# Kernel tuning notes

Measured on AMD Instinct MI355X. Metric: run time of the kernel, lower is better.

## Reference

```python
import jax, jax.numpy as jnp
import numpy as np

NEG_BIG = -1e38

def setup_inputs() -> dict:
    key = jax.random.key(0)
    kq, kk, kv, kwq, kwk = jax.random.split(key, 5)
    B, S, d_model, d_k, d_v = 4, 4096, 256, 64, 64
    return {
        "q": jax.random.normal(kq, (B, S, d_model), dtype=jnp.float32),
        "k": jax.random.normal(kk, (B, S, d_model), dtype=jnp.float32),
        "v": jax.random.normal(kv, (B, S, d_v), dtype=jnp.float32),
        "w_q": jax.random.normal(kwq, (d_k, d_model), dtype=jnp.float32) * 0.01,
        "w_k": jax.random.normal(kwk, (d_k, d_model), dtype=jnp.float32) * 0.01,
    }

def reference(q, k, v, w_q, w_k):
    d_k = w_q.shape[0]
    temperature = jnp.asarray(np.power(d_k, 0.5), dtype=q.dtype)
    # relu-projected Q, K: [B,S,d_k]
    qp = jax.nn.relu(jnp.einsum("bsm,km->bsk", q, w_q))
    kp = jax.nn.relu(jnp.einsum("bsm,km->bsk", k, w_k))
    # scores [B,S,S]
    attn = jnp.einsum("bqd,bkd->bqk", qp, kp) / temperature
    # force column 0 to -1e38 (inline custom mask)
    attn = attn.at[:, :, 0].set(NEG_BIG)
    attn = jax.nn.softmax(attn, axis=2)
    # dropout is identity in eval / p=0
    out = jnp.einsum("bqk,bkd->bqd", attn, v)
    return out
```

## Files before the change

### kernel.cpp

```cpp
#include <hip/hip_runtime.h>

#define B_    4
#define S_    4096
#define DM    256
#define DK    64
#define NROWS (B_ * S_)
#define LOG2E 1.4426950408889634f
#define PACK_BIAS 0.0028151295f

typedef __attribute__((ext_vector_type(8))) short bfrag;
typedef __attribute__((ext_vector_type(4))) float ffrag;

__device__ __forceinline__ unsigned bf16_rne_hi(float x) {
    unsigned u = __float_as_uint(x);
    return u + 0x7fffu + ((u >> 16) & 1u);
}
__device__ __forceinline__ unsigned short f2bf(float x) {
    return (unsigned short)(bf16_rne_hi(x) >> 16);
}
__device__ __forceinline__ unsigned pack_bf16x2(float lo, float hi) {
    return (bf16_rne_hi(hi) & 0xffff0000u) | (bf16_rne_hi(lo) >> 16);
}

__device__ __forceinline__ float fast_exp2(float x) {
#if __has_builtin(__builtin_amdgcn_exp2f)
    return __builtin_amdgcn_exp2f(x);
#else
    float r;
    asm("v_exp_f32 %0, %1\n\ts_nop 1" : "=v"(r) : "v"(x));
    return r;
#endif
}

__device__ __forceinline__ unsigned trunc_pack_bf16x2(float lo, float hi) {
    return __builtin_amdgcn_perm(__float_as_uint(hi), __float_as_uint(lo),
                                 0x07060302u);
}

__global__ __launch_bounds__(256) void fused_prep(
    const float* __restrict__ q, const float* __restrict__ k,
    const float* __restrict__ v, const float* __restrict__ wq,
    const float* __restrict__ wk, unsigned short* __restrict__ vT,
    unsigned short* __restrict__ qpb, unsigned short* __restrict__ kpb)
{
    __shared__ __align__(16) char smem[64 * 264 * 2];
    const int blk  = blockIdx.x;
    const int lane = threadIdx.x & 63, w = threadIdx.x >> 6;

    if (blk < 256) {
        float (*tile)[65] = (float(*)[65])smem;
        const int b = blk >> 6, s0 = (blk & 63) * 64;
#pragma unroll
        for (int i = 0; i < 16; ++i) {
            const int sl = i * 4 + w;
            tile[sl][lane] = v[(b * S_ + s0 + sl) * DK + lane];
        }
        __syncthreads();
        const int t32 = lane >> 5, pos = lane & 31;
        const int keyl = t32 * 32 + ((pos & 1) ? (pos >> 1) + 16 : (pos >> 1));
#pragma unroll
        for (int i = 0; i < 16; ++i) {
            const int d = i * 4 + w;
            vT[((size_t)(b * 128 + (s0 >> 5) + t32) * 64 + d) * 32 + pos] =
                f2bf(tile[keyl][d]);
        }
    } else {
        unsigned short* wlds = (unsigned short*)smem;
        const int pb = blk - 256;
        const int half = pb >> 8, rblk = pb & 255;
        const float* x;
        const float* wsrc;
        unsigned short* o;
        float scale;
        if (half == 0) { x = q; wsrc = wq; o = qpb; scale = 0.125f * LOG2E; }
        else           { x = k; wsrc = wk; o = kpb; scale = 1.0f; }

#pragma unroll
        for (int i = 0; i < 16; ++i) {
            const int idx4 = i * 256 + threadIdx.x;
            const int r = idx4 >> 6, c4 = idx4 & 63;
            const float4 wv = ((const float4*)wsrc)[idx4];
            uint2 pk;
            pk.x = pack_bf16x2(wv.x, wv.y);
            pk.y = pack_bf16x2(wv.z, wv.w);
            *(uint2*)&wlds[r * 264 + c4 * 4] = pk;
        }
        __syncthreads();

        const int m = lane & 15, quad = lane >> 4;
        const int rows0 = rblk * 64 + w * 16;
        const float* xrow = x + (size_t)(rows0 + m) * DM + quad * 8;

        ffrag acc[4];
#pragma unroll
        for (int dt = 0; dt < 4; ++dt) acc[dt] = (ffrag)(0.0f);

        float4 xb[2][2];
        xb[0][0] = ((const float4*)xrow)[0];
        xb[0][1] = ((const float4*)xrow)[1];

#pragma unroll 2
        for (int kf = 0; kf < 8; ++kf) {
            const int p = kf & 1;
            if (kf < 7) {
                const float4* xn = (const float4*)(xrow + (kf + 1) * 32);
                xb[p ^ 1][0] = xn[0];
                xb[p ^ 1][1] = xn[1];
            }
            union { bfrag v; unsigned u[4]; } pk;
            pk.u[0] = pack_bf16x2(xb[p][0].x, xb[p][0].y);
            pk.u[1] = pack_bf16x2(xb[p][0].z, xb[p][0].w);
            pk.u[2] = pack_bf16x2(xb[p][1].x, xb[p][1].y);
            pk.u[3] = pack_bf16x2(xb[p][1].z, xb[p][1].w);
#pragma unroll
            for (int dt = 0; dt < 4; ++dt) {
                const bfrag Bf = *(const bfrag*)&wlds[(dt * 16 + m) * 264 + kf * 32 + quad * 8];
                acc[dt] = __builtin_amdgcn_mfma_f32_16x16x32_bf16(pk.v, Bf, acc[dt], 0, 0, 0);
            }
        }
#pragma unroll
        for (int dt = 0; dt < 4; ++dt)
#pragma unroll
            for (int r = 0; r < 4; ++r)
                o[(rows0 + quad * 4 + r) * DK + dt * 16 + m] =
                    f2bf(fmaxf(acc[dt][r], 0.0f) * scale);
    }
}

__global__ __launch_bounds__(256) void attn_mfma(
    const unsigned short* __restrict__ qp, const unsigned short* __restrict__ kp,
    const unsigned short* __restrict__ vT, float* __restrict__ num_part,
    float* __restrict__ den_part)
{
    __shared__ __align__(16) char smem[20480];
    unsigned short* Plds = (unsigned short*)smem;
    float* red0 = (float*)smem;
    float* red1 = (float*)smem + 2560;

    const int lane = threadIdx.x & 63, w = threadIdx.x >> 6;
    const int m = lane & 15, quad = lane >> 4;

    const int flat = blockIdx.x;
    const int wid  = ((flat & 7) << 7) | (flat >> 3);
    const int gy   = wid & 1;
    const int qg   = wid >> 1;

    const int qbase = qg * 32;
    const int b = qg >> 7;
    const int kstart = (gy * 4 + w) * 512;

    bfrag qa[2][2];
#pragma unroll
    for (int mt = 0; mt < 2; ++mt)
#pragma unroll
        for (int kf = 0; kf < 2; ++kf)
            qa[mt][kf] = *(const bfrag*)&qp[(qbase + mt * 16 + m) * DK + kf * 32 + quad * 8];

    ffrag oacc[2][4];
    float dacc[2][4];
#pragma unroll
    for (int mt = 0; mt < 2; ++mt) {
#pragma unroll
        for (int dt = 0; dt < 4; ++dt) oacc[mt][dt] = (ffrag)(0.0f);
#pragma unroll
        for (int r = 0; r < 4; ++r) dacc[mt][r] = 0.0f;
    }

    const unsigned short* kptr = kp + ((size_t)b * S_ + kstart + m) * DK + quad * 8;
    const unsigned short* vptr = vT + ((size_t)(b * 128 + (kstart >> 5)) * 64 + m) * 32 + quad * 8;
    unsigned short* Pw = Plds + w * 1280;

    const ffrag cbias = (ffrag)(PACK_BIAS);

    bfrag kbuf[2][2][2], vbuf[2][4];
#pragma unroll
    for (int kt = 0; kt < 2; ++kt)
#pragma unroll
        for (int kf = 0; kf < 2; ++kf)
            kbuf[0][kt][kf] = *(const bfrag*)(kptr + kt * 1024 + kf * 32);
#pragma unroll
    for (int dt = 0; dt < 4; ++dt)
        vbuf[0][dt] = *(const bfrag*)(vptr + dt * 512);

    bfrag pa0, pa1;

#pragma unroll 2
    for (int jj = 0; jj < 16; ++jj) {
        const int p = jj & 1;

        if (jj < 15) {
            const unsigned short* kn = kptr + (jj + 1) * 2048;
#pragma unroll
            for (int kt = 0; kt < 2; ++kt)
#pragma unroll
                for (int kf = 0; kf < 2; ++kf)
                    kbuf[p ^ 1][kt][kf] = *(const bfrag*)(kn + kt * 1024 + kf * 32);
        }

        if (jj > 0) {
#pragma unroll
            for (int dt = 0; dt < 4; ++dt) {
                oacc[0][dt] = __builtin_amdgcn_mfma_f32_16x16x32_bf16(pa0, vbuf[p ^ 1][dt], oacc[0][dt], 0, 0, 0);
                oacc[1][dt] = __builtin_amdgcn_mfma_f32_16x16x32_bf16(pa1, vbuf[p ^ 1][dt], oacc[1][dt], 0, 0, 0);
            }
        }

        if (jj < 15) {
            const unsigned short* vn = vptr + (jj + 1) * 2048;
#pragma unroll
            for (int dt = 0; dt < 4; ++dt)
                vbuf[p ^ 1][dt] = *(const bfrag*)(vn + dt * 512);
        }

        ffrag s[2][2];
#pragma unroll
        for (int mt = 0; mt < 2; ++mt)
#pragma unroll
            for (int kt = 0; kt < 2; ++kt) {
                ffrag t = __builtin_amdgcn_mfma_f32_16x16x32_bf16(qa[mt][0], kbuf[p][kt][0], cbias, 0, 0, 0);
                s[mt][kt] = __builtin_amdgcn_mfma_f32_16x16x32_bf16(qa[mt][1], kbuf[p][kt][1], t, 0, 0, 0);
            }

        const bool mask0 = (jj == 0) && (kstart == 0) && (m == 0);
#pragma unroll
        for (int mt = 0; mt < 2; ++mt)
#pragma unroll
            for (int r = 0; r < 4; ++r) {
                float e0 = fast_exp2(s[mt][0][r]);
                float e1 = fast_exp2(s[mt][1][r]);
                if (mask0) e0 = 0.0f;
                dacc[mt][r] += e0 + e1;
                *(unsigned*)&Pw[(mt * 16 + quad * 4 + r) * 40 + m * 2] =
                    trunc_pack_bf16x2(e0, e1);
            }

        pa0 = *(const bfrag*)&Pw[(m) * 40 + quad * 8];
        pa1 = *(const bfrag*)&Pw[(16 + m) * 40 + quad * 8];
    }
#pragma unroll
    for (int dt = 0; dt < 4; ++dt) {
        oacc[0][dt] = __builtin_amdgcn_mfma_f32_16x16x32_bf16(pa0, vbuf[1][dt], oacc[0][dt], 0, 0, 0);
        oacc[1][dt] = __builtin_amdgcn_mfma_f32_16x16x32_bf16(pa1, vbuf[1][dt], oacc[1][dt], 0, 0, 0);
    }

#pragma unroll
    for (int mt = 0; mt < 2; ++mt)
#pragma unroll
        for (int r = 0; r < 4; ++r) {
            float d = dacc[mt][r];
            d += __shfl_xor(d, 1, 64);
            d += __shfl_xor(d, 2, 64);
            d += __shfl_xor(d, 4, 64);
            d += __shfl_xor(d, 8, 64);
            dacc[mt][r] = d;
        }

    __syncthreads();
    float* red[2] = { red0, red1 };
    if (w >= 2) {
#pragma unroll
        for (int mt = 0; mt < 2; ++mt) {
#pragma unroll
            for (int dt = 0; dt < 4; ++dt)
#pragma unroll
                for (int r = 0; r < 4; ++r)
                    red[w - 2][((mt * 4 + dt) * 4 + r) * 64 + lane] = oacc[mt][dt][r];
#pragma unroll
            for (int r = 0; r < 4; ++r)
                red[w - 2][2048 + (mt * 4 + r) * 64 + lane] = dacc[mt][r];
        }
    }
    __syncthreads();
    if (w < 2) {
#pragma unroll
        for (int mt = 0; mt < 2; ++mt) {
#pragma unroll
            for (int dt = 0; dt < 4; ++dt)
#pragma unroll
                for (int r = 0; r < 4; ++r)
                    oacc[mt][dt][r] += red[w][((mt * 4 + dt) * 4 + r) * 64 + lane];
#pragma unroll
            for (int r = 0; r < 4; ++r)
                dacc[mt][r] += red[w][2048 + (mt * 4 + r) * 64 + lane];
        }
    }
    __syncthreads();
    if (w == 1) {
#pragma unroll
        for (int mt = 0; mt < 2; ++mt) {
#pragma unroll
            for (int dt = 0; dt < 4; ++dt)
#pragma unroll
                for (int r = 0; r < 4; ++r)
                    red0[((mt * 4 + dt) * 4 + r) * 64 + lane] = oacc[mt][dt][r];
#pragma unroll
            for (int r = 0; r < 4; ++r)
                red0[2048 + (mt * 4 + r) * 64 + lane] = dacc[mt][r];
        }
    }
    __syncthreads();
    if (w == 0) {
#pragma unroll
        for (int mt = 0; mt < 2; ++mt) {
#pragma unroll
            for (int dt = 0; dt < 4; ++dt)
#pragma unroll
                for (int r = 0; r < 4; ++r) {
                    const float nv = oacc[mt][dt][r] + red0[((mt * 4 + dt) * 4 + r) * 64 + lane];
                    num_part[(size_t)gy * NROWS * DK +
                             (qbase + mt * 16 + quad * 4 + r) * DK + dt * 16 + m] = nv;
                }
#pragma unroll
            for (int r = 0; r < 4; ++r) {
                const float dv = dacc[mt][r] + red0[2048 + (mt * 4 + r) * 64 + lane];
                if (m == 0)
                    den_part[gy * NROWS + qbase + mt * 16 + quad * 4 + r] = dv;
            }
        }
    }
}

__global__ __launch_bounds__(256) void finalize_kernel(
    const float* __restrict__ num_part, const float* __restrict__ den_part,
    float* __restrict__ out)
{
    const int i4 = blockIdx.x * 256 + threadIdx.x;
    const int row = i4 >> 4;
    const float4 a = ((const float4*)num_part)[i4];
    const float4 c = ((const float4*)(num_part + (size_t)NROWS * DK))[i4];
    const float inv = 1.0f / (den_part[row] + den_part[NROWS + row]);
    float4 o;
    o.x = (a.x + c.x) * inv;
    o.y = (a.y + c.y) * inv;
    o.z = (a.z + c.z) * inv;
    o.w = (a.w + c.w) * inv;
    ((float4*)out)[i4] = o;
}

extern "C" void kernel_launch(void* const* d_in, const int* in_sizes, int n_in,
                              void* d_out, int out_size, void* d_ws, size_t ws_size,
                              hipStream_t stream)
{
    const float* q  = (const float*)d_in[0];
    const float* k  = (const float*)d_in[1];
    const float* v  = (const float*)d_in[2];
    const float* wq = (const float*)d_in[3];
    const float* wk = (const float*)d_in[4];
    float* out = (float*)d_out;

    char* p = (char*)d_ws;
    unsigned short* qpb = (unsigned short*)p;   p += (size_t)NROWS * DK * 2;
    unsigned short* kpb = (unsigned short*)p;   p += (size_t)NROWS * DK * 2;
    unsigned short* vT  = (unsigned short*)p;   p += (size_t)B_ * DK * S_ * 2;
    float* num_part     = (float*)p;            p += (size_t)2 * NROWS * DK * 4;
    float* den_part     = (float*)p;

    fused_prep<<<768, 256, 0, stream>>>(q, k, v, wq, wk, vT, qpb, kpb);
    attn_mfma<<<1024, 256, 0, stream>>>(qpb, kpb, vT, num_part, den_part);
    finalize_kernel<<<NROWS * DK / 4 / 256, 256, 0, stream>>>(num_part, den_part, out);
}
```

Before: 136.1 us.

## Fuse prep, attention and finalize into one cooperative kernel with grid syncs

Merges the three kernel launches into a single cooperative kernel of 1024 blocks that uses grid-wide syncs between the projection/transpose, attention and finalize phases. The goal is to remove launch gaps and tail effects between kernels. The projection phase also now issues all x loads ahead of the weight staging so global latency overlaps with the LDS fill. In exchange, the whole grid must be co-resident (4 blocks per CU), the attention phase runs with the larger shared allocation and a register bound, and the grid syncs add barrier cost. The old three-kernel path is kept as a fallback.

```diff
diff --git a/kernel.cpp b/kernel.cpp
--- a/kernel.cpp
+++ b/kernel.cpp
@@ -1,4 +1,7 @@
 #include <hip/hip_runtime.h>
+#include <hip/hip_cooperative_groups.h>
+
+namespace cg = cooperative_groups;
 
 #define B_    4
 #define S_    4096
@@ -37,110 +40,122 @@
                                  0x07060302u);
 }
 
-__global__ __launch_bounds__(256) void fused_prep(
+__device__ __forceinline__ void phase_transpose(
+    char* smem, int blk, int tid,
+    const float* __restrict__ v, unsigned short* __restrict__ vT)
+{
+    float (*tile)[65] = (float(*)[65])smem;
+    const int lane = tid & 63, w = tid >> 6;
+    const int b = blk >> 6, s0 = (blk & 63) * 64;
+#pragma unroll
+    for (int i = 0; i < 16; ++i) {
+        const int sl = i * 4 + w;
+        tile[sl][lane] = v[(b * S_ + s0 + sl) * DK + lane];
+    }
+    __syncthreads();
+    const int t32 = lane >> 5, pos = lane & 31;
+    const int keyl = t32 * 32 + ((pos & 1) ? (pos >> 1) + 16 : (pos >> 1));
+#pragma unroll
+    for (int i = 0; i < 16; ++i) {
+        const int d = i * 4 + w;
+        vT[((size_t)(b * 128 + (s0 >> 5) + t32) * 64 + d) * 32 + pos] =
+            f2bf(tile[keyl][d]);
+    }
+}
+
+__device__ __forceinline__ void proj_step(
+    const float4 xv0, const float4 xv1, const unsigned short* wlds,
+    int kf, int m, int quad, ffrag acc[4])
+{
+    union { bfrag v; unsigned u[4]; } pk;
+    pk.u[0] = pack_bf16x2(xv0.x, xv0.y);
+    pk.u[1] = pack_bf16x2(xv0.z, xv0.w);
+    pk.u[2] = pack_bf16x2(xv1.x, xv1.y);
+    pk.u[3] = pack_bf16x2(xv1.z, xv1.w);
+#pragma unroll
+    for (int dt = 0; dt < 4; ++dt) {
+        const bfrag Bf = *(const bfrag*)&wlds[(dt * 16 + m) * 264 + kf * 32 + quad * 8];
+        acc[dt] = __builtin_amdgcn_mfma_f32_16x16x32_bf16(pk.v, Bf, acc[dt], 0, 0, 0);
+    }
+}
+
+__device__ __forceinline__ void phase_proj(
+    char* smem, int blk, int tid,
     const float* __restrict__ q, const float* __restrict__ k,
-    const float* __restrict__ v, const float* __restrict__ wq,
-    const float* __restrict__ wk, unsigned short* __restrict__ vT,
+    const float* __restrict__ wq, const float* __restrict__ wk,
     unsigned short* __restrict__ qpb, unsigned short* __restrict__ kpb)
 {
-    __shared__ __align__(16) char smem[64 * 264 * 2];
-    const int blk  = blockIdx.x;
-    const int lane = threadIdx.x & 63, w = threadIdx.x >> 6;
-
-    if (blk < 256) {
-        float (*tile)[65] = (float(*)[65])smem;
-        const int b = blk >> 6, s0 = (blk & 63) * 64;
-#pragma unroll
-        for (int i = 0; i < 16; ++i) {
-            const int sl = i * 4 + w;
-            tile[sl][lane] = v[(b * S_ + s0 + sl) * DK + lane];
-        }
-        __syncthreads();
-        const int t32 = lane >> 5, pos = lane & 31;
-        const int keyl = t32 * 32 + ((pos & 1) ? (pos >> 1) + 16 : (pos >> 1));
-#pragma unroll
-        for (int i = 0; i < 16; ++i) {
-            const int d = i * 4 + w;
-            vT[((size_t)(b * 128 + (s0 >> 5) + t32) * 64 + d) * 32 + pos] =
-                f2bf(tile[keyl][d]);
-        }
-    } else {
-        unsigned short* wlds = (unsigned short*)smem;
-        const int pb = blk - 256;
-        const int half = pb >> 8, rblk = pb & 255;
-        const float* x;
-        const float* wsrc;
-        unsigned short* o;
-        float scale;
-        if (half == 0) { x = q; wsrc = wq; o = qpb; scale = 0.125f * LOG2E; }
-        else           { x = k; wsrc = wk; o = kpb; scale = 1.0f; }
-
-#pragma unroll
-        for (int i = 0; i < 16; ++i) {
-            const int idx4 = i * 256 + threadIdx.x;
-            const int r = idx4 >> 6, c4 = idx4 & 63;
-            const float4 wv = ((const float4*)wsrc)[idx4];
-            uint2 pk;
-            pk.x = pack_bf16x2(wv.x, wv.y);
-            pk.y = pack_bf16x2(wv.z, wv.w);
-            *(uint2*)&wlds[r * 264 + c4 * 4] = pk;
-        }
-        __syncthreads();
-
-        const int m = lane & 15, quad = lane >> 4;
-        const int rows0 = rblk * 64 + w * 16;
-        const float* xrow = x + (size_t)(rows0 + m) * DM + quad * 8;
-
-        ffrag acc[4];
-#pragma unroll
-        for (int dt = 0; dt < 4; ++dt) acc[dt] = (ffrag)(0.0f);
-
-        float4 xb[2][2];
-        xb[0][0] = ((const float4*)xrow)[0];
-        xb[0][1] = ((const float4*)xrow)[1];
-
-#pragma unroll 2
-        for (int kf = 0; kf < 8; ++kf) {
-            const int p = kf & 1;
-            if (kf < 7) {
-                const float4* xn = (const float4*)(xrow + (kf + 1) * 32);
-                xb[p ^ 1][0] = xn[0];
-                xb[p ^ 1][1] = xn[1];
-            }
-            union { bfrag v; unsigned u[4]; } pk;
-            pk.u[0] = pack_bf16x2(xb[p][0].x, xb[p][0].y);
-            pk.u[1] = pack_bf16x2(xb[p][0].z, xb[p][0].w);
-            pk.u[2] = pack_bf16x2(xb[p][1].x, xb[p][1].y);
-            pk.u[3] = pack_bf16x2(xb[p][1].z, xb[p][1].w);
-#pragma unroll
-            for (int dt = 0; dt < 4; ++dt) {
-                const bfrag Bf = *(const bfrag*)&wlds[(dt * 16 + m) * 264 + kf * 32 + quad * 8];
-                acc[dt] = __builtin_amdgcn_mfma_f32_16x16x32_bf16(pk.v, Bf, acc[dt], 0, 0, 0);
-            }
-        }
-#pragma unroll
-        for (int dt = 0; dt < 4; ++dt)
-#pragma unroll
-            for (int r = 0; r < 4; ++r)
-                o[(rows0 + quad * 4 + r) * DK + dt * 16 + m] =
-                    f2bf(fmaxf(acc[dt][r], 0.0f) * scale);
-    }
-}
-
-__global__ __launch_bounds__(256) void attn_mfma(
+    unsigned short* wlds = (unsigned short*)smem;
+    const int lane = tid & 63, w = tid >> 6;
+    const int pb = blk - 256;
+    const int half = pb >> 8, rblk = pb & 255;
+    const float* x;
+    const float* wsrc;
+    unsigned short* o;
+    float scale;
+    if (half == 0) { x = q; wsrc = wq; o = qpb; scale = 0.125f * LOG2E; }
+    else           { x = k; wsrc = wk; o = kpb; scale = 1.0f; }
+
+    const int m = lane & 15, quad = lane >> 4;
+    const int rows0 = rblk * 64 + w * 16;
+    const float* xrow = x + (size_t)(rows0 + m) * DM + quad * 8;
+    const float4* xf4 = (const float4*)xrow;
+
+    float4 xA[4][2];
+#pragma unroll
+    for (int t = 0; t < 4; ++t) {
+        xA[t][0] = xf4[t * 8];
+        xA[t][1] = xf4[t * 8 + 1];
+    }
+
+#pragma unroll
+    for (int i = 0; i < 16; ++i) {
+        const int idx4 = i * 256 + tid;
+        const int r = idx4 >> 6, c4 = idx4 & 63;
+        const float4 wv = ((const float4*)wsrc)[idx4];
+        uint2 pk;
+        pk.x = pack_bf16x2(wv.x, wv.y);
+        pk.y = pack_bf16x2(wv.z, wv.w);
+        *(uint2*)&wlds[r * 264 + c4 * 4] = pk;
+    }
+    __syncthreads();
+
+    ffrag acc[4];
+#pragma unroll
+    for (int dt = 0; dt < 4; ++dt) acc[dt] = (ffrag)(0.0f);
+
+    float4 xB[4][2];
+#pragma unroll
+    for (int kf = 0; kf < 4; ++kf) {
+        xB[kf][0] = xf4[(kf + 4) * 8];
+        xB[kf][1] = xf4[(kf + 4) * 8 + 1];
+        proj_step(xA[kf][0], xA[kf][1], wlds, kf, m, quad, acc);
+    }
+#pragma unroll
+    for (int kf = 0; kf < 4; ++kf)
+        proj_step(xB[kf][0], xB[kf][1], wlds, kf + 4, m, quad, acc);
+
+#pragma unroll
+    for (int dt = 0; dt < 4; ++dt)
+#pragma unroll
+        for (int r = 0; r < 4; ++r)
+            o[(rows0 + quad * 4 + r) * DK + dt * 16 + m] =
+                f2bf(fmaxf(acc[dt][r], 0.0f) * scale);
+}
+
+__device__ __forceinline__ void phase_attn(
+    char* smem, int flat, int tid,
     const unsigned short* __restrict__ qp, const unsigned short* __restrict__ kp,
     const unsigned short* __restrict__ vT, float* __restrict__ num_part,
     float* __restrict__ den_part)
 {
-    __shared__ __align__(16) char smem[20480];
     unsigned short* Plds = (unsigned short*)smem;
     float* red0 = (float*)smem;
     float* red1 = (float*)smem + 2560;
 
-    const int lane = threadIdx.x & 63, w = threadIdx.x >> 6;
+    const int lane = tid & 63, w = tid >> 6;
     const int m = lane & 15, quad = lane >> 4;
 
-    const int flat = blockIdx.x;
     const int wid  = ((flat & 7) << 7) | (flat >> 3);
     const int gy   = wid & 1;
     const int qg   = wid >> 1;
@@ -320,11 +335,11 @@
     }
 }
 
-__global__ __launch_bounds__(256) void finalize_kernel(
-    const float* __restrict__ num_part, const float* __restrict__ den_part,
-    float* __restrict__ out)
-{
-    const int i4 = blockIdx.x * 256 + threadIdx.x;
+__device__ __forceinline__ void phase_finalize(
+    int blk, int tid, const float* __restrict__ num_part,
+    const float* __restrict__ den_part, float* __restrict__ out)
+{
+    const int i4 = blk * 256 + tid;
     const int row = i4 >> 4;
     const float4 a = ((const float4*)num_part)[i4];
     const float4 c = ((const float4*)(num_part + (size_t)NROWS * DK))[i4];
@@ -337,6 +352,58 @@
     ((float4*)out)[i4] = o;
 }
 
+__global__ __launch_bounds__(256, 4) void fused_all(
+    const float* __restrict__ q, const float* __restrict__ k,
+    const float* __restrict__ v, const float* __restrict__ wq,
+    const float* __restrict__ wk, unsigned short* __restrict__ vT,
+    unsigned short* __restrict__ qpb, unsigned short* __restrict__ kpb,
+    float* __restrict__ num_part, float* __restrict__ den_part,
+    float* __restrict__ out)
+{
+    __shared__ __align__(16) char smem[64 * 264 * 2];
+    const int blk = blockIdx.x, tid = threadIdx.x;
+    cg::grid_group grid = cg::this_grid();
+
+    if (blk < 256)      phase_transpose(smem, blk, tid, v, vT);
+    else if (blk < 768) phase_proj(smem, blk, tid, q, k, wq, wk, qpb, kpb);
+
+    grid.sync();
+
+    phase_attn(smem, blk, tid, qpb, kpb, vT, num_part, den_part);
+
+    grid.sync();
+
+    phase_finalize(blk, tid, num_part, den_part, out);
+}
+
+__global__ __launch_bounds__(256) void fused_prep(
+    const float* __restrict__ q, const float* __restrict__ k,
+    const float* __restrict__ v, const float* __restrict__ wq,
+    const float* __restrict__ wk, unsigned short* __restrict__ vT,
+    unsigned short* __restrict__ qpb, unsigned short* __restrict__ kpb)
+{
+    __shared__ __align__(16) char smem[64 * 264 * 2];
+    const int blk = blockIdx.x, tid = threadIdx.x;
+    if (blk < 256) phase_transpose(smem, blk, tid, v, vT);
+    else           phase_proj(smem, blk, tid, q, k, wq, wk, qpb, kpb);
+}
+
+__global__ __launch_bounds__(256) void attn_mfma(
+    const unsigned short* __restrict__ qp, const unsigned short* __restrict__ kp,
+    const unsigned short* __restrict__ vT, float* __restrict__ num_part,
+    float* __restrict__ den_part)
+{
+    __shared__ __align__(16) char smem[20480];
+    phase_attn(smem, blockIdx.x, threadIdx.x, qp, kp, vT, num_part, den_part);
+}
+
+__global__ __launch_bounds__(256) void finalize_kernel(
+    const float* __restrict__ num_part, const float* __restrict__ den_part,
+    float* __restrict__ out)
+{
+    phase_finalize(blockIdx.x, threadIdx.x, num_part, den_part, out);
+}
+
 extern "C" void kernel_launch(void* const* d_in, const int* in_sizes, int n_in,
                               void* d_out, int out_size, void* d_ws, size_t ws_size,
                               hipStream_t stream)
@@ -355,6 +422,24 @@
     float* num_part     = (float*)p;            p += (size_t)2 * NROWS * DK * 4;
     float* den_part     = (float*)p;
 
+    static int coop = -1;
+    if (coop < 0) {
+        int nb = 0;
+        hipError_t e = hipOccupancyMaxActiveBlocksPerMultiprocessor(
+            &nb, (const void*)fused_all, 256, 0);
+        coop = (e == hipSuccess && nb >= 4) ? 1 : 0;
+    }
+
+    if (coop) {
+        void* args[] = { (void*)&q, (void*)&k, (void*)&v, (void*)&wq, (void*)&wk,
+                         (void*)&vT, (void*)&qpb, (void*)&kpb,
+                         (void*)&num_part, (void*)&den_part, (void*)&out };
+        hipError_t e = hipLaunchCooperativeKernel(
+            (const void*)fused_all, dim3(1024), dim3(256), args, 0, stream);
+        if (e == hipSuccess) return;
+        coop = 0;
+    }
+
     fused_prep<<<768, 256, 0, stream>>>(q, k, v, wq, wk, vT, qpb, kpb);
     attn_mfma<<<1024, 256, 0, stream>>>(qpb, kpb, vT, num_part, den_part);
     finalize_kernel<<<NROWS * DK / 4 / 256, 256, 0, stream>>>(num_part, den_part, out);
```

Measured after the change: 137.8 us. Within noise of the previous version (+1.2%).

## Deepen K prefetch to three buffers and front-load projection input loads

Applied to the files above, without the earlier changes.

In the attention kernel, K tiles now go into a three-slot ring with a prefetch distance of two iterations. The QK^T MFMAs are moved ahead of the previous tile's PV MFMAs, and the key loop is fully unrolled so the ring indices are compile-time constants. In the projection kernel, each thread's first half of x rows is loaded before the weight tile is staged into LDS, and the second half is loaded while the first half feeds the MFMAs. The goal is to hide global-load latency behind compute, at the cost of more registers and larger code.

```diff
diff --git a/kernel.cpp b/kernel.cpp
--- a/kernel.cpp
+++ b/kernel.cpp
@@ -37,6 +37,22 @@
                                  0x07060302u);
 }
 
+__device__ __forceinline__ void proj_step(
+    const float4 xv0, const float4 xv1, const unsigned short* wlds,
+    int kf, int m, int quad, ffrag acc[4])
+{
+    union { bfrag v; unsigned u[4]; } pk;
+    pk.u[0] = pack_bf16x2(xv0.x, xv0.y);
+    pk.u[1] = pack_bf16x2(xv0.z, xv0.w);
+    pk.u[2] = pack_bf16x2(xv1.x, xv1.y);
+    pk.u[3] = pack_bf16x2(xv1.z, xv1.w);
+#pragma unroll
+    for (int dt = 0; dt < 4; ++dt) {
+        const bfrag Bf = *(const bfrag*)&wlds[(dt * 16 + m) * 264 + kf * 32 + quad * 8];
+        acc[dt] = __builtin_amdgcn_mfma_f32_16x16x32_bf16(pk.v, Bf, acc[dt], 0, 0, 0);
+    }
+}
+
 __global__ __launch_bounds__(256) void fused_prep(
     const float* __restrict__ q, const float* __restrict__ k,
     const float* __restrict__ v, const float* __restrict__ wq,
@@ -45,7 +61,8 @@
 {
     __shared__ __align__(16) char smem[64 * 264 * 2];
     const int blk  = blockIdx.x;
-    const int lane = threadIdx.x & 63, w = threadIdx.x >> 6;
+    const int tid  = threadIdx.x;
+    const int lane = tid & 63, w = tid >> 6;
 
     if (blk < 256) {
         float (*tile)[65] = (float(*)[65])smem;
@@ -75,9 +92,21 @@
         if (half == 0) { x = q; wsrc = wq; o = qpb; scale = 0.125f * LOG2E; }
         else           { x = k; wsrc = wk; o = kpb; scale = 1.0f; }
 
+        const int m = lane & 15, quad = lane >> 4;
+        const int rows0 = rblk * 64 + w * 16;
+        const float* xrow = x + (size_t)(rows0 + m) * DM + quad * 8;
+        const float4* xf4 = (const float4*)xrow;
+
+        float4 xA[4][2];
+#pragma unroll
+        for (int t = 0; t < 4; ++t) {
+            xA[t][0] = xf4[t * 8];
+            xA[t][1] = xf4[t * 8 + 1];
+        }
+
 #pragma unroll
         for (int i = 0; i < 16; ++i) {
-            const int idx4 = i * 256 + threadIdx.x;
+            const int idx4 = i * 256 + tid;
             const int r = idx4 >> 6, c4 = idx4 & 63;
             const float4 wv = ((const float4*)wsrc)[idx4];
             uint2 pk;
@@ -87,37 +116,21 @@
         }
         __syncthreads();
 
-        const int m = lane & 15, quad = lane >> 4;
-        const int rows0 = rblk * 64 + w * 16;
-        const float* xrow = x + (size_t)(rows0 + m) * DM + quad * 8;
-
         ffrag acc[4];
 #pragma unroll
         for (int dt = 0; dt < 4; ++dt) acc[dt] = (ffrag)(0.0f);
 
-        float4 xb[2][2];
-        xb[0][0] = ((const float4*)xrow)[0];
-        xb[0][1] = ((const float4*)xrow)[1];
-
-#pragma unroll 2
-        for (int kf = 0; kf < 8; ++kf) {
-            const int p = kf & 1;
-            if (kf < 7) {
-                const float4* xn = (const float4*)(xrow + (kf + 1) * 32);
-                xb[p ^ 1][0] = xn[0];
-                xb[p ^ 1][1] = xn[1];
-            }
-            union { bfrag v; unsigned u[4]; } pk;
-            pk.u[0] = pack_bf16x2(xb[p][0].x, xb[p][0].y);
-            pk.u[1] = pack_bf16x2(xb[p][0].z, xb[p][0].w);
-            pk.u[2] = pack_bf16x2(xb[p][1].x, xb[p][1].y);
-            pk.u[3] = pack_bf16x2(xb[p][1].z, xb[p][1].w);
-#pragma unroll
-            for (int dt = 0; dt < 4; ++dt) {
-                const bfrag Bf = *(const bfrag*)&wlds[(dt * 16 + m) * 264 + kf * 32 + quad * 8];
-                acc[dt] = __builtin_amdgcn_mfma_f32_16x16x32_bf16(pk.v, Bf, acc[dt], 0, 0, 0);
-            }
-        }
+        float4 xB[4][2];
+#pragma unroll
+        for (int kf = 0; kf < 4; ++kf) {
+            xB[kf][0] = xf4[(kf + 4) * 8];
+            xB[kf][1] = xf4[(kf + 4) * 8 + 1];
+            proj_step(xA[kf][0], xA[kf][1], wlds, kf, m, quad, acc);
+        }
+#pragma unroll
+        for (int kf = 0; kf < 4; ++kf)
+            proj_step(xB[kf][0], xB[kf][1], wlds, kf + 4, m, quad, acc);
+
 #pragma unroll
         for (int dt = 0; dt < 4; ++dt)
 #pragma unroll
@@ -172,30 +185,45 @@
 
     const ffrag cbias = (ffrag)(PACK_BIAS);
 
-    bfrag kbuf[2][2][2], vbuf[2][4];
-#pragma unroll
-    for (int kt = 0; kt < 2; ++kt)
-#pragma unroll
-        for (int kf = 0; kf < 2; ++kf)
-            kbuf[0][kt][kf] = *(const bfrag*)(kptr + kt * 1024 + kf * 32);
-#pragma unroll
-    for (int dt = 0; dt < 4; ++dt)
-        vbuf[0][dt] = *(const bfrag*)(vptr + dt * 512);
+    bfrag kbuf[3][2][2], vbuf[2][4];
+#pragma unroll
+    for (int s = 0; s < 2; ++s) {
+        const unsigned short* kn = kptr + s * 2048;
+#pragma unroll
+        for (int kt = 0; kt < 2; ++kt)
+#pragma unroll
+            for (int kf = 0; kf < 2; ++kf)
+                kbuf[s][kt][kf] = *(const bfrag*)(kn + kt * 1024 + kf * 32);
+#pragma unroll
+        for (int dt = 0; dt < 4; ++dt)
+            vbuf[s][dt] = *(const bfrag*)(vptr + s * 2048 + dt * 512);
+    }
 
     bfrag pa0, pa1;
 
-#pragma unroll 2
+#pragma unroll
     for (int jj = 0; jj < 16; ++jj) {
         const int p = jj & 1;
-
-        if (jj < 15) {
-            const unsigned short* kn = kptr + (jj + 1) * 2048;
+        const int ks  = jj % 3;
+        const int ks2 = (jj + 2) % 3;
+
+        if (jj < 14) {
+            const unsigned short* kn = kptr + (jj + 2) * 2048;
 #pragma unroll
             for (int kt = 0; kt < 2; ++kt)
 #pragma unroll
                 for (int kf = 0; kf < 2; ++kf)
-                    kbuf[p ^ 1][kt][kf] = *(const bfrag*)(kn + kt * 1024 + kf * 32);
-        }
+                    kbuf[ks2][kt][kf] = *(const bfrag*)(kn + kt * 1024 + kf * 32);
+        }
+
+        ffrag s[2][2];
+#pragma unroll
+        for (int mt = 0; mt < 2; ++mt)
+#pragma unroll
+            for (int kt = 0; kt < 2; ++kt) {
+                ffrag t = __builtin_amdgcn_mfma_f32_16x16x32_bf16(qa[mt][0], kbuf[ks][kt][0], cbias, 0, 0, 0);
+                s[mt][kt] = __builtin_amdgcn_mfma_f32_16x16x32_bf16(qa[mt][1], kbuf[ks][kt][1], t, 0, 0, 0);
+            }
 
         if (jj > 0) {
 #pragma unroll
@@ -211,15 +239,6 @@
             for (int dt = 0; dt < 4; ++dt)
                 vbuf[p ^ 1][dt] = *(const bfrag*)(vn + dt * 512);
         }
-
-        ffrag s[2][2];
-#pragma unroll
-        for (int mt = 0; mt < 2; ++mt)
-#pragma unroll
-            for (int kt = 0; kt < 2; ++kt) {
-                ffrag t = __builtin_amdgcn_mfma_f32_16x16x32_bf16(qa[mt][0], kbuf[p][kt][0], cbias, 0, 0, 0);
-                s[mt][kt] = __builtin_amdgcn_mfma_f32_16x16x32_bf16(qa[mt][1], kbuf[p][kt][1], t, 0, 0, 0);
-            }
 
         const bool mask0 = (jj == 0) && (kstart == 0) && (m == 0);
 #pragma unroll
```

New measurement: 172.4 us. +26.6%, slower.
